# Optimization experiments

Measured on AMD Instinct MI355X. Metric: run time of the kernel, lower is better.

## Reference

```python
import jax, jax.numpy as jnp
import numpy as np


def fps(x, k):
    """Farthest point sampling. x: [B, N, D]. Returns int32 indices [B, k].
    Deterministic: first selected point is index 0 (torch repo uses randint init;
    we fix 0 for a reproducible baseline)."""
    B, N, D = x.shape
    binds = jnp.arange(B)

    def step(carry, _):
        dist, far = carry                      # dist: [B, N], far: [B]
        centroid = x[binds, far]               # [B, D]
        d = jnp.sum((x - centroid[:, None, :]) ** 2, axis=-1)  # [B, N]
        dist = jnp.minimum(dist, d)
        nxt = jnp.argmax(dist, axis=-1)
        return (dist, nxt), far

    init = (jnp.full((B, N), jnp.inf, dtype=x.dtype),
            jnp.zeros((B,), dtype=jnp.int32))
    _, idxs = jax.lax.scan(step, init, None, length=k)
    return idxs.T                              # [B, k]


def sine_mlp(x, params, w0=1.0):
    """Stack of 1x1 convs (== per-point linear) with sin(w0*.) activations.
    x: [B, N, C_in] -> [B, N, C_out]."""
    h = x
    for W, b in params:                        # W: [C_out, C_in], b: [C_out]
        h = jnp.sin(w0 * (jnp.einsum('bnc,oc->bno', h, W) + b))
    return h


_DIMS = [(6, 32), (32, 64), (64, 64), (64, 128), (128, 256), (256, 512)]


def setup_inputs() -> dict:
    key = jax.random.key(0)
    keys = jax.random.split(key, 1 + 2 * len(_DIMS))
    inp = {"x": jax.random.normal(keys[0], (16, 8192, 6), dtype=jnp.float32)}
    for i, (cin, cout) in enumerate(_DIMS):
        scale = 1.0 / np.sqrt(cin)
        inp[f"W{i+1}"] = jax.random.normal(keys[1 + 2 * i], (cout, cin), dtype=jnp.float32) * scale
        inp[f"b{i+1}"] = jax.random.normal(keys[2 + 2 * i], (cout,), dtype=jnp.float32) * 0.01
    inp["k"] = 1024
    return inp


def reference(x, W1, b1, W2, b2, W3, b3, W4, b4, W5, b5, W6, b6, k):
    params = [(W1, b1), (W2, b2), (W3, b3), (W4, b4), (W5, b5), (W6, b6)]
    sample_idx = fps(x, k)                     # [B, k] int32
    feat = sine_mlp(x, params)                 # [B, N, 512]
    # index_points gather along point dim, then permute back -> [B, k, 512]
    out = jnp.take_along_axis(feat, sample_idx[:, :, None], axis=1)
    return out
```

## Files before the change

kernel.cpp:

```cpp
#include <hip/hip_runtime.h>
#include <hip/hip_bf16.h>

#define NPTS 8192
#define KS   1024
#define NB   16

__global__ __launch_bounds__(1024, 4)
__attribute__((amdgpu_waves_per_eu(4, 4)))
void fps_kernel(const float* __restrict__ x, int* __restrict__ idx_out) {
#pragma clang fp contract(off)
  const int b    = blockIdx.x;
  const int tid  = threadIdx.x;
  const int lane = tid & 63;
  const int wave = tid >> 6;
  const float* xb = x + (size_t)b * NPTS * 6;

  float ca[48];
  {
    const float4* src = reinterpret_cast<const float4*>(xb + tid * 48);
    #pragma unroll
    for (int i = 0; i < 12; ++i) {
      float4 v = src[i];
      asm volatile("v_accvgpr_write_b32 %0, %1" : "=a"(ca[4*i+0]) : "v"(v.x));
      asm volatile("v_accvgpr_write_b32 %0, %1" : "=a"(ca[4*i+1]) : "v"(v.y));
      asm volatile("v_accvgpr_write_b32 %0, %1" : "=a"(ca[4*i+2]) : "v"(v.z));
      asm volatile("v_accvgpr_write_b32 %0, %1" : "=a"(ca[4*i+3]) : "v"(v.w));
    }
  }

  float dist[8];
  #pragma unroll
  for (int j = 0; j < 8; ++j) dist[j] = __builtin_huge_valf();

  __shared__ uint2 wvi[2][16];

  if (tid == 0) idx_out[b * KS] = 0;
  int bi = 0;

  for (int step = 0; step < KS - 1; ++step) {
    const float* cp = xb + bi * 6;
    const float c0 = cp[0], c1 = cp[1], c2 = cp[2],
                c3 = cp[3], c4 = cp[4], c5 = cp[5];

    float bestv = -1.0f;
    int   besti = 0;
    #pragma unroll
    for (int j = 0; j < 8; ++j) {
      float xv[6];
      #pragma unroll
      for (int d = 0; d < 6; ++d)
        asm volatile("v_accvgpr_read_b32 %0, %1" : "=v"(xv[d]) : "a"(ca[6*j+d]));
      float t0 = xv[0] - c0; float s = t0 * t0;
      float t1 = xv[1] - c1; s = s + t1 * t1;
      float t2 = xv[2] - c2; s = s + t2 * t2;
      float t3 = xv[3] - c3; s = s + t3 * t3;
      float t4 = xv[4] - c4; s = s + t4 * t4;
      float t5 = xv[5] - c5; s = s + t5 * t5;
      float nd = fminf(dist[j], s);
      dist[j] = nd;
      if (nd > bestv) { bestv = nd; besti = tid * 8 + j; }
    }

    float wmax = bestv;
    #pragma unroll
    for (int off = 1; off < 64; off <<= 1)
      wmax = fmaxf(wmax, __shfl_xor(wmax, off, 64));
    unsigned long long ball = __ballot(bestv == wmax);
    int wlane = (int)__builtin_ctzll(ball);
    int widx  = __builtin_amdgcn_readlane(besti, wlane);

    if (lane == 0) wvi[step & 1][wave] = make_uint2((unsigned)widx, __float_as_uint(wmax));
    __syncthreads();

    uint2 wr = wvi[step & 1][lane & 15];
    float cv = __uint_as_float(wr.y);
    #pragma unroll
    for (int off = 1; off < 16; off <<= 1)
      cv = fmaxf(cv, __shfl_xor(cv, off, 64));
    unsigned long long b2 = __ballot(__uint_as_float(wr.y) == cv);
    int cl = (int)__builtin_ctzll(b2);
    bi = __builtin_amdgcn_readlane((int)wr.x, cl);

    if (tid == 0) idx_out[b * KS + step + 1] = bi;
  }
}

template<int NT, int JP, int CINP, int CINT, int COUT, int CT, bool LAST>
__device__ __forceinline__ void run_layer(const float* __restrict__ W,
                                          const float* __restrict__ bias,
                                          const float* __restrict__ in,
                                          float* __restrict__ outlds,
                                          float* __restrict__ gout,
                                          float* __restrict__ wt,
                                          int qbase, int tid) {
  constexpr int S = (COUT + 63) / 64;
  const int lane = tid & 63;
  const int wave = tid >> 6;
  const int p0   = wave * JP;

  float acc[JP][S];
  {
    float bv[S];
    #pragma unroll
    for (int s = 0; s < S; ++s) {
      int o = s * 64 + lane;
      bv[s] = (o < COUT) ? bias[o] : 0.f;
    }
    #pragma unroll
    for (int j = 0; j < JP; ++j)
      #pragma unroll
      for (int s = 0; s < S; ++s) acc[j][s] = bv[s];
  }

  for (int ct0 = 0; ct0 < CINT; ct0 += CT) {
    __syncthreads();
    #pragma unroll 1
    for (int e = tid; e < COUT * CT; e += NT) {
      int o  = e / CT;
      int cc = e % CT;
      wt[cc * (COUT + 1) + o] = W[o * CINT + ct0 + cc];
    }
    __syncthreads();
    #pragma unroll
    for (int cc0 = 0; cc0 < CT; cc0 += 4) {
      if (CT - cc0 >= 4) {
        float a[JP][4];
        #pragma unroll
        for (int j = 0; j < JP; ++j) {
          float4 t = *reinterpret_cast<const float4*>(&in[(p0 + j) * CINP + ct0 + cc0]);
          a[j][0] = t.x; a[j][1] = t.y; a[j][2] = t.z; a[j][3] = t.w;
        }
        #pragma unroll
        for (int u = 0; u < 4; ++u) {
          float wvv[S];
          #pragma unroll
          for (int s = 0; s < S; ++s)
            wvv[s] = wt[(cc0 + u) * (COUT + 1) + s * 64 + lane];
          #pragma unroll
          for (int j = 0; j < JP; ++j)
            #pragma unroll
            for (int s = 0; s < S; ++s)
              acc[j][s] = fmaf(a[j][u], wvv[s], acc[j][s]);
        }
      } else {
        float a[JP][2];
        #pragma unroll
        for (int j = 0; j < JP; ++j) {
          float2 t = *reinterpret_cast<const float2*>(&in[(p0 + j) * CINP + ct0 + cc0]);
          a[j][0] = t.x; a[j][1] = t.y;
        }
        #pragma unroll
        for (int u = 0; u < 2; ++u) {
          float wvv[S];
          #pragma unroll
          for (int s = 0; s < S; ++s)
            wvv[s] = wt[(cc0 + u) * (COUT + 1) + s * 64 + lane];
          #pragma unroll
          for (int j = 0; j < JP; ++j)
            #pragma unroll
            for (int s = 0; s < S; ++s)
              acc[j][s] = fmaf(a[j][u], wvv[s], acc[j][s]);
        }
      }
    }
  }
  #pragma unroll
  for (int j = 0; j < JP; ++j) {
    #pragma unroll
    for (int s = 0; s < S; ++s) {
      int o = s * 64 + lane;
      if (o < COUT) {
        float r = sinf(acc[j][s]);
        if (LAST) gout[(size_t)(qbase + p0 + j) * 512 + o] = r;
        else      outlds[(p0 + j) * COUT + o] = r;
      }
    }
  }
}

__global__ __launch_bounds__(1024, 4) void mlp_kernel(
    const float* __restrict__ x, const int* __restrict__ sidx,
    const float* __restrict__ W1, const float* __restrict__ B1,
    const float* __restrict__ W2, const float* __restrict__ B2,
    const float* __restrict__ W3, const float* __restrict__ B3,
    const float* __restrict__ W4, const float* __restrict__ B4,
    const float* __restrict__ W5, const float* __restrict__ B5,
    const float* __restrict__ W6, const float* __restrict__ B6,
    float* __restrict__ out) {
  __shared__ float A[64 * 128];
  __shared__ float Bb[64 * 256];
  __shared__ float wt[16 * 513];
  const int tid   = threadIdx.x;
  const int qbase = blockIdx.x * 64;

  if (tid < 64) {
    int q  = qbase + tid;
    int bb = q >> 10;
    int id = sidx[q];
    const float* xr = x + ((size_t)bb * NPTS + id) * 6;
    #pragma unroll
    for (int d = 0; d < 6; ++d) A[tid * 8 + d] = xr[d];
  }
  run_layer<1024, 4, 8,   6,  32,  6, false>(W1, B1, A,  Bb, nullptr, wt, qbase, tid);
  run_layer<1024, 4, 32,  32,  64, 16, false>(W2, B2, Bb, A,  nullptr, wt, qbase, tid);
  run_layer<1024, 4, 64,  64,  64, 16, false>(W3, B3, A,  Bb, nullptr, wt, qbase, tid);
  run_layer<1024, 4, 64,  64, 128, 16, false>(W4, B4, Bb, A,  nullptr, wt, qbase, tid);
  run_layer<1024, 4, 128, 128, 256, 16, false>(W5, B5, A,  Bb, nullptr, wt, qbase, tid);
  run_layer<1024, 4, 256, 256, 512, 16, true >(W6, B6, Bb, nullptr, out, wt, qbase, tid);
}

extern "C" void kernel_launch(void* const* d_in, const int* in_sizes, int n_in,
                              void* d_out, int out_size, void* d_ws, size_t ws_size,
                              hipStream_t stream) {
  const float* x  = (const float*)d_in[0];
  const float* W1 = (const float*)d_in[1];  const float* B1 = (const float*)d_in[2];
  const float* W2 = (const float*)d_in[3];  const float* B2 = (const float*)d_in[4];
  const float* W3 = (const float*)d_in[5];  const float* B3 = (const float*)d_in[6];
  const float* W4 = (const float*)d_in[7];  const float* B4 = (const float*)d_in[8];
  const float* W5 = (const float*)d_in[9];  const float* B5 = (const float*)d_in[10];
  const float* W6 = (const float*)d_in[11]; const float* B6 = (const float*)d_in[12];
  int*   idxbuf = (int*)d_ws;
  float* out    = (float*)d_out;

  fps_kernel<<<NB, 1024, 0, stream>>>(x, idxbuf);
  mlp_kernel<<<256, 1024, 0, stream>>>(x, idxbuf,
                                       W1, B1, W2, B2, W3, B3,
                                       W4, B4, W5, B5, W6, B6, out);
}
```

Baseline: 2.202 ms.

## Split FPS per batch across 16 blocks with global atomic step handshake

Farthest point sampling now spreads each batch over 16 workgroups of 256 threads, each holding 2 points in registers, instead of one 1024-thread block with 8 points per thread. The per-step argmax packs value, inverted index and a step tag into one 64-bit key, so a single integer max reduction suffices. Blocks publish their partial max to global slots with release stores and spin-poll the other slots with acquire loads until the step tag matches. This shortens each step's per-thread distance work and reduction chain, at the cost of a cross-CU handshake every step. It relies on all 256 blocks being co-resident and on uninitialised workspace slots not matching a step tag.

```diff
diff --git a/kernel.cpp b/kernel.cpp
--- a/kernel.cpp
+++ b/kernel.cpp
@@ -5,36 +5,35 @@
 #define KS   1024
 #define NB   16
 
-__global__ __launch_bounds__(1024, 4)
-__attribute__((amdgpu_waves_per_eu(4, 4)))
-void fps_kernel(const float* __restrict__ x, int* __restrict__ idx_out) {
+__global__ __launch_bounds__(256, 1)
+void fps_kernel(const float* __restrict__ x, int* __restrict__ idx_out,
+                unsigned long long* __restrict__ slots) {
 #pragma clang fp contract(off)
-  const int b    = blockIdx.x;
+  const int blk  = blockIdx.x;
+  const int b    = blk >> 4;
+  const int part = blk & 15;
   const int tid  = threadIdx.x;
   const int lane = tid & 63;
   const int wave = tid >> 6;
   const float* xb = x + (size_t)b * NPTS * 6;
-
-  float ca[48];
+  const int p0   = part * 512 + tid * 2;
+
+  float crd[12];
   {
-    const float4* src = reinterpret_cast<const float4*>(xb + tid * 48);
-    #pragma unroll
-    for (int i = 0; i < 12; ++i) {
+    const float4* src = reinterpret_cast<const float4*>(xb + (size_t)p0 * 6);
+    #pragma unroll
+    for (int i = 0; i < 3; ++i) {
       float4 v = src[i];
-      asm volatile("v_accvgpr_write_b32 %0, %1" : "=a"(ca[4*i+0]) : "v"(v.x));
-      asm volatile("v_accvgpr_write_b32 %0, %1" : "=a"(ca[4*i+1]) : "v"(v.y));
-      asm volatile("v_accvgpr_write_b32 %0, %1" : "=a"(ca[4*i+2]) : "v"(v.z));
-      asm volatile("v_accvgpr_write_b32 %0, %1" : "=a"(ca[4*i+3]) : "v"(v.w));
-    }
-  }
-
-  float dist[8];
-  #pragma unroll
-  for (int j = 0; j < 8; ++j) dist[j] = __builtin_huge_valf();
-
-  __shared__ uint2 wvi[2][16];
-
-  if (tid == 0) idx_out[b * KS] = 0;
+      crd[4*i+0] = v.x; crd[4*i+1] = v.y; crd[4*i+2] = v.z; crd[4*i+3] = v.w;
+    }
+  }
+  float d0 = __builtin_huge_valf(), d1 = __builtin_huge_valf();
+
+  unsigned long long* bsl = slots + b * 16;
+  __shared__ unsigned long long ws4[4];
+  __shared__ unsigned long long gws;
+
+  if (part == 0 && tid == 0) idx_out[b * KS] = 0;
   int bi = 0;
 
   for (int step = 0; step < KS - 1; ++step) {
@@ -42,46 +41,68 @@
     const float c0 = cp[0], c1 = cp[1], c2 = cp[2],
                 c3 = cp[3], c4 = cp[4], c5 = cp[5];
 
-    float bestv = -1.0f;
-    int   besti = 0;
-    #pragma unroll
-    for (int j = 0; j < 8; ++j) {
-      float xv[6];
+    float bestv; int besti;
+    {
+      float t0 = crd[0] - c0; float s = t0 * t0;
+      float t1 = crd[1] - c1; s = s + t1 * t1;
+      float t2 = crd[2] - c2; s = s + t2 * t2;
+      float t3 = crd[3] - c3; s = s + t3 * t3;
+      float t4 = crd[4] - c4; s = s + t4 * t4;
+      float t5 = crd[5] - c5; s = s + t5 * t5;
+      d0 = fminf(d0, s);
+      bestv = d0; besti = p0;
+    }
+    {
+      float t0 = crd[6]  - c0; float s = t0 * t0;
+      float t1 = crd[7]  - c1; s = s + t1 * t1;
+      float t2 = crd[8]  - c2; s = s + t2 * t2;
+      float t3 = crd[9]  - c3; s = s + t3 * t3;
+      float t4 = crd[10] - c4; s = s + t4 * t4;
+      float t5 = crd[11] - c5; s = s + t5 * t5;
+      d1 = fminf(d1, s);
+      if (d1 > bestv) { bestv = d1; besti = p0 + 1; }
+    }
+
+    unsigned long long pk = ((unsigned long long)__float_as_uint(bestv) << 32)
+                          | ((unsigned long long)((~besti) & 0x1FFF) << 19)
+                          | (unsigned long long)(step + 1);
+    #pragma unroll
+    for (int off = 1; off < 64; off <<= 1) {
+      unsigned long long o = __shfl_xor(pk, off, 64);
+      if (o > pk) pk = o;
+    }
+    if (lane == 0) ws4[wave] = pk;
+    __syncthreads();
+    unsigned long long bw = ws4[lane & 3];
+    #pragma unroll
+    for (int off = 1; off < 4; off <<= 1) {
+      unsigned long long o = __shfl_xor(bw, off, 64);
+      if (o > bw) bw = o;
+    }
+    if (tid == 0)
+      __hip_atomic_store(&bsl[part], bw, __ATOMIC_RELEASE, __HIP_MEMORY_SCOPE_AGENT);
+    if (wave == 0) {
+      unsigned long long r = 0;
+      if (lane < 16) {
+        if (lane == part) {
+          r = bw;
+        } else {
+          do {
+            r = __hip_atomic_load(&bsl[lane], __ATOMIC_ACQUIRE, __HIP_MEMORY_SCOPE_AGENT);
+          } while ((unsigned)(r & 0x7FFFFull) != (unsigned)(step + 1));
+        }
+      }
       #pragma unroll
-      for (int d = 0; d < 6; ++d)
-        asm volatile("v_accvgpr_read_b32 %0, %1" : "=v"(xv[d]) : "a"(ca[6*j+d]));
-      float t0 = xv[0] - c0; float s = t0 * t0;
-      float t1 = xv[1] - c1; s = s + t1 * t1;
-      float t2 = xv[2] - c2; s = s + t2 * t2;
-      float t3 = xv[3] - c3; s = s + t3 * t3;
-      float t4 = xv[4] - c4; s = s + t4 * t4;
-      float t5 = xv[5] - c5; s = s + t5 * t5;
-      float nd = fminf(dist[j], s);
-      dist[j] = nd;
-      if (nd > bestv) { bestv = nd; besti = tid * 8 + j; }
-    }
-
-    float wmax = bestv;
-    #pragma unroll
-    for (int off = 1; off < 64; off <<= 1)
-      wmax = fmaxf(wmax, __shfl_xor(wmax, off, 64));
-    unsigned long long ball = __ballot(bestv == wmax);
-    int wlane = (int)__builtin_ctzll(ball);
-    int widx  = __builtin_amdgcn_readlane(besti, wlane);
-
-    if (lane == 0) wvi[step & 1][wave] = make_uint2((unsigned)widx, __float_as_uint(wmax));
-    __syncthreads();
-
-    uint2 wr = wvi[step & 1][lane & 15];
-    float cv = __uint_as_float(wr.y);
-    #pragma unroll
-    for (int off = 1; off < 16; off <<= 1)
-      cv = fmaxf(cv, __shfl_xor(cv, off, 64));
-    unsigned long long b2 = __ballot(__uint_as_float(wr.y) == cv);
-    int cl = (int)__builtin_ctzll(b2);
-    bi = __builtin_amdgcn_readlane((int)wr.x, cl);
-
-    if (tid == 0) idx_out[b * KS + step + 1] = bi;
+      for (int off = 1; off < 16; off <<= 1) {
+        unsigned long long o = __shfl_xor(r, off, 64);
+        if (o > r) r = o;
+      }
+      if (lane == 0) gws = r;
+    }
+    __syncthreads();
+    const unsigned long long w = gws;
+    bi = (int)__builtin_amdgcn_readfirstlane((unsigned)((~(w >> 19)) & 0x1FFF));
+    if (part == 0 && tid == 0) idx_out[b * KS + step + 1] = bi;
   }
 }
 
@@ -219,10 +240,12 @@
   const float* W4 = (const float*)d_in[7];  const float* B4 = (const float*)d_in[8];
   const float* W5 = (const float*)d_in[9];  const float* B5 = (const float*)d_in[10];
   const float* W6 = (const float*)d_in[11]; const float* B6 = (const float*)d_in[12];
-  int*   idxbuf = (int*)d_ws;
-  float* out    = (float*)d_out;
-
-  fps_kernel<<<NB, 1024, 0, stream>>>(x, idxbuf);
+
+  unsigned long long* slots = (unsigned long long*)d_ws;
+  int* idxbuf = (int*)((char*)d_ws + 4096);
+  float* out  = (float*)d_out;
+
+  fps_kernel<<<256, 256, 0, stream>>>(x, idxbuf, slots);
   mlp_kernel<<<256, 1024, 0, stream>>>(x, idxbuf,
                                        W1, B1, W2, B2, W3, B3,
                                        W4, B4, W5, B5, W6, B6, out);
```

After: 5.405 ms. 2.45x slower.
